# Optimization experiments

Hardware: AMD Instinct MI355X
Metric: run time of the kernel (lower is better)

## Reference

```python
import jax, jax.numpy as jnp
import numpy as np

DIM = 768; DEPTH = 4; HEADS = 12; DHEAD = 64; INNER = HEADS * DHEAD; FF = 4 * DIM
CHUNK = 64; ROTD = 32  # rotary_emb_dim = max(dim_head//2, 32); freqs dim = ROTD (16 freqs duplicated)
B = 2; N = 2048; K = 32; R = 2; CN = 128


def _rotary(seq_len, offset=0):
    inv_freq = 1.0 / (10000.0 ** (jnp.arange(0, ROTD, 2, dtype=jnp.float32) / ROTD))
    pos = jnp.arange(seq_len, dtype=jnp.float32) + offset
    fr = pos[:, None] * inv_freq[None, :]
    return jnp.concatenate([fr, fr], axis=-1)  # (seq_len, ROTD)


def _rope(t, freqs):
    # t: (b, h, n, DHEAD); freqs: (n, rd). Rotate first rd dims, pass the rest.
    rd = freqs.shape[-1]
    t1, t2 = t[..., :rd], t[..., rd:]
    half = rd // 2
    rot = jnp.concatenate([-t1[..., half:], t1[..., :half]], axis=-1)
    return jnp.concatenate([t1 * jnp.cos(freqs) + rot * jnp.sin(freqs), t2], axis=-1)


def _rmsnorm(x, gamma, eps=1e-8):
    n = jnp.linalg.norm(x, axis=-1, keepdims=True) * (x.shape[-1] ** -0.5)
    return x / jnp.maximum(n, eps) * gamma


def _attn(x, gamma, wq, wkv, wo, bo, q_freqs, k_freqs, causal, context=None, mask=None):
    xn = _rmsnorm(x, gamma)
    kv_in = xn if context is None else context
    b = x.shape[0]
    q = (xn @ wq).reshape(b, -1, HEADS, DHEAD).transpose(0, 2, 1, 3)
    k, v = jnp.split(kv_in @ wkv, 2, axis=-1)
    k = k.reshape(b, -1, HEADS, DHEAD).transpose(0, 2, 1, 3)
    v = v.reshape(b, -1, HEADS, DHEAD).transpose(0, 2, 1, 3)
    q = q * (DHEAD ** -0.5)
    q = _rope(q, q_freqs)
    k = _rope(k, k_freqs)
    sim = jnp.einsum('bhid,bhjd->bhij', q, k)
    neg = -jnp.finfo(sim.dtype).max
    if mask is not None:
        sim = jnp.where(mask[:, None, None, :], sim, neg)
    if causal:
        i, j = sim.shape[-2], sim.shape[-1]
        cm = jnp.arange(j)[None, :] > (jnp.arange(i)[:, None] + (j - i))
        sim = jnp.where(cm, neg, sim)
    attn = jax.nn.softmax(sim, axis=-1)
    out = jnp.einsum('bhij,bhjd->bhid', attn, v)
    out = out.transpose(0, 2, 1, 3).reshape(b, -1, INNER)
    return out @ wo + bo


def _forward(x, retrieved, context_mask, attn_gamma, attn_wq, attn_wkv, attn_wo, attn_bo,
             ca_gamma, ca_wq, ca_wkv, ca_wo, ca_bo, ff_gamma, ff_w1, ff_b1, ff_w2, ff_b2, final_gamma):
    b, n = x.shape[0], x.shape[1]
    k_chunks, r, cn = retrieved.shape[1], retrieved.shape[2], retrieved.shape[3]
    seq_chunk = n // k_chunks  # == CHUNK
    pad = CHUNK - 1

    self_freqs = _rotary(n)
    # cross-attn q pos emb: rotary(seq_chunk, offset=CHUNK-1) then F.pad (-pad, pad)
    qf = _rotary(seq_chunk, offset=pad)
    qf = jnp.concatenate([qf[pad:], jnp.zeros((pad, ROTD), qf.dtype)], axis=0)  # (seq_chunk, ROTD)
    kf = jnp.tile(_rotary(cn), (r, 1))  # (r*cn, ROTD)

    ctx = retrieved.reshape(b * k_chunks, r * cn, DIM)
    cmask = context_mask.reshape(b * k_chunks, r * cn)

    for l in range(DEPTH):
        # causal self-attention with RoPE
        x = _attn(x, attn_gamma[l], attn_wq[l], attn_wkv[l], attn_wo[l], attn_bo[l],
                  self_freqs, self_freqs, True) + x
        # chunked cross-attention
        xs = jnp.concatenate([x[:, pad:], jnp.zeros((b, pad, DIM), x.dtype)], axis=1)
        xs = xs.reshape(b * k_chunks, seq_chunk, DIM)
        co = _attn(xs, ca_gamma[l], ca_wq[l], ca_wkv[l], ca_wo[l], ca_bo[l],
                   qf, kf, False, context=ctx, mask=cmask)
        co = co.reshape(b, n, DIM)
        co = jnp.concatenate([jnp.zeros((b, pad, DIM), co.dtype), co[:, :-pad]], axis=1)
        x = co + x
        # feed-forward (RMSNorm -> Linear -> GELU -> Linear)
        h = _rmsnorm(x, ff_gamma[l])
        h = jax.nn.gelu(h @ ff_w1[l] + ff_b1[l], approximate=False)
        x = (h @ ff_w2[l] + ff_b2[l]) + x

    return _rmsnorm(x, final_gamma)


def setup_inputs() -> dict:
    key = jax.random.key(0)
    ks = jax.random.split(key, 16)
    s = 0.02
    inp = {
        'x': jax.random.normal(ks[0], (B, N, DIM), jnp.float32),
        'retrieved': jax.random.normal(ks[1], (B, K, R, CN, DIM), jnp.float32),
        'context_mask': jnp.ones((B, K, R, CN), jnp.bool_),
        'attn_gamma': jnp.ones((DEPTH, DIM), jnp.float32),
        'attn_wq': s * jax.random.normal(ks[2], (DEPTH, DIM, INNER), jnp.float32),
        'attn_wkv': s * jax.random.normal(ks[3], (DEPTH, DIM, 2 * INNER), jnp.float32),
        'attn_wo': s * jax.random.normal(ks[4], (DEPTH, INNER, DIM), jnp.float32),
        'attn_bo': jnp.zeros((DEPTH, DIM), jnp.float32),
        'ca_gamma': jnp.ones((DEPTH, DIM), jnp.float32),
        'ca_wq': s * jax.random.normal(ks[5], (DEPTH, DIM, INNER), jnp.float32),
        'ca_wkv': s * jax.random.normal(ks[6], (DEPTH, DIM, 2 * INNER), jnp.float32),
        'ca_wo': s * jax.random.normal(ks[7], (DEPTH, INNER, DIM), jnp.float32),
        'ca_bo': jnp.zeros((DEPTH, DIM), jnp.float32),
        'ff_gamma': jnp.ones((DEPTH, DIM), jnp.float32),
        'ff_w1': s * jax.random.normal(ks[8], (DEPTH, DIM, FF), jnp.float32),
        'ff_b1': jnp.zeros((DEPTH, FF), jnp.float32),
        'ff_w2': s * jax.random.normal(ks[9], (DEPTH, FF, DIM), jnp.float32),
        'ff_b2': jnp.zeros((DEPTH, DIM), jnp.float32),
        'final_gamma': jnp.ones((DIM,), jnp.float32),
    }
    return inp


def reference(x, retrieved, context_mask, attn_gamma, attn_wq, attn_wkv, attn_wo, attn_bo,
              ca_gamma, ca_wq, ca_wkv, ca_wo, ca_bo, ff_gamma, ff_w1, ff_b1, ff_w2, ff_b2, final_gamma):
    return _forward(x, retrieved, context_mask, attn_gamma, attn_wq, attn_wkv, attn_wo, attn_bo,
                    ca_gamma, ca_wq, ca_wkv, ca_wo, ca_bo, ff_gamma, ff_w1, ff_b1, ff_w2, ff_b2, final_gamma)
```

## Files before the change

kernel.cpp:

```cpp
#include <hip/hip_runtime.h>


#define DIM 768
#define DEPTH 4
#define HEADS 12
#define DHEAD 64
#define INNER 768
#define FF 3072
#define NSEQ 2048
#define BB 2
#define NROWS 4096
#define CTXROWS 16384
#define PAD 63

typedef __attribute__((ext_vector_type(4))) float f32x4;
typedef __attribute__((ext_vector_type(16))) float f32x16;
typedef __attribute__((ext_vector_type(8))) short bf16x8;
typedef unsigned short ushort_t;

__device__ __forceinline__ ushort_t f2bf(float f) {
    union { float f; unsigned u; } c; c.f = f;
    unsigned r = c.u + 0x7fffu + ((c.u >> 16) & 1u);
    return (ushort_t)(r >> 16);
}
__device__ __forceinline__ float bf2f(ushort_t u) {
    return __uint_as_float(((unsigned)u) << 16);
}
__device__ __forceinline__ unsigned cvt_pk_bf16(float lo, float hi) {
    unsigned r;
    asm("v_cvt_pk_bf16_f32 %0, %1, %2" : "=v"(r) : "v"(lo), "v"(hi));
    return r;
}

__device__ __forceinline__ void gload16(const ushort_t* g, ushort_t* l) {
    __builtin_amdgcn_global_load_lds(
        (const __attribute__((address_space(1))) unsigned int*)g,
        (__attribute__((address_space(3))) unsigned int*)l,
        16, 0, 0);
}

__global__ __launch_bounds__(256) void f32_to_bf16_kernel(
    const float* __restrict__ in, ushort_t* __restrict__ out, long n)
{
    long i = ((long)blockIdx.x * 256 + threadIdx.x) * 4;
    if (i + 3 < n) {
        float4 v = *(const float4*)(in + i);
        unsigned long long pk =
            (unsigned long long)f2bf(v.x)
          | ((unsigned long long)f2bf(v.y) << 16)
          | ((unsigned long long)f2bf(v.z) << 32)
          | ((unsigned long long)f2bf(v.w) << 48);
        *(unsigned long long*)(out + i) = pk;
    }
}

__global__ __launch_bounds__(256) void rope_tab_kernel(float2* __restrict__ tbl)
{
    int idx = blockIdx.x * 256 + threadIdx.x;
    int pos = idx >> 4, dd = idx & 15;
    float inv = __expf(-(float)dd * 0.57564627324851f);
    float f = (float)pos * inv;
    float sn, cs;
    sincosf(f, &sn, &cs);
    tbl[idx] = make_float2(cs, sn);
}

__global__ __launch_bounds__(256) void transpose_all_kernel(
    const float* __restrict__ wq,  const float* __restrict__ wkv,
    const float* __restrict__ wo,  const float* __restrict__ cawq,
    const float* __restrict__ cawkv, const float* __restrict__ cawo,
    const float* __restrict__ w1,  const float* __restrict__ w2,
    ushort_t* __restrict__ WT, size_t perLayer)
{
    const size_t szQ = 768ULL * 768, szKV = 768ULL * 1536, szW1 = 768ULL * 3072;
    int t = blockIdx.x, l = blockIdx.y;
    const float* src; int K, N; size_t dstOff; int rel;
    if      (t < 576)  { src = wq;    K = 768;  N = 768;  dstOff = 0;                 rel = t; }
    else if (t < 1728) { src = wkv;   K = 768;  N = 1536; dstOff = szQ;               rel = t - 576; }
    else if (t < 2304) { src = wo;    K = 768;  N = 768;  dstOff = szQ + szKV;        rel = t - 1728; }
    else if (t < 2880) { src = cawq;  K = 768;  N = 768;  dstOff = szQ*2 + szKV;      rel = t - 2304; }
    else if (t < 4032) { src = cawkv; K = 768;  N = 1536; dstOff = szQ*3 + szKV;      rel = t - 2880; }
    else if (t < 4608) { src = cawo;  K = 768;  N = 768;  dstOff = szQ*3 + szKV*2;    rel = t - 4032; }
    else if (t < 6912) { src = w1;    K = 768;  N = 3072; dstOff = szQ*4 + szKV*2;    rel = t - 4608; }
    else               { src = w2;    K = 3072; N = 768;  dstOff = szQ*4 + szKV*2 + szW1; rel = t - 6912; }
    src += (size_t)l * K * N;
    ushort_t* dst = WT + (size_t)l * perLayer + dstOff;
    int tx = N >> 5;
    int bx = (rel % tx) * 32;
    int by = (rel / tx) * 32;

    __shared__ float tile[32][33];
    int cx = threadIdx.x & 31, cy = threadIdx.x >> 5;
    #pragma unroll
    for (int i = 0; i < 32; i += 8)
        tile[cy + i][cx] = src[(long)(by + cy + i) * N + bx + cx];
    __syncthreads();
    #pragma unroll
    for (int i = 0; i < 32; i += 8)
        dst[(long)(bx + cy + i) * K + by + cx] = f2bf(tile[cx][cy + i]);
}

__global__ __launch_bounds__(256) void vtrans_kernel(
    const ushort_t* __restrict__ src, long srcStride, long vOff,
    ushort_t* __restrict__ VT, int kPG)
{
    __shared__ __align__(16) ushort_t tile[64][72];
    const int rt = blockIdx.x;
    const int h = blockIdx.y;
    const int row0 = rt * 64;
    const int g = row0 / kPG;
    const int kb = row0 % kPG;
    const int t = threadIdx.x;
    const int r = t >> 2, q4 = (t & 3) * 16;

    const ushort_t* s = src + (long)(row0 + r) * srcStride + vOff + h * DHEAD + q4;
    *(uint4*)&tile[r][q4]     = *(const uint4*)s;
    *(uint4*)&tile[r][q4 + 8] = *(const uint4*)(s + 8);
    __syncthreads();

    ushort_t tmp[16];
    #pragma unroll
    for (int c = 0; c < 16; c++) tmp[c] = tile[q4 + c][r];
    ushort_t* dst = VT + (((long)(g * HEADS + h) * DHEAD + r) * kPG + kb + q4);
    *(uint4*)dst       = *(uint4*)&tmp[0];
    *(uint4*)(dst + 8) = *(uint4*)&tmp[8];
}

template<int MODE>
__global__ __launch_bounds__(256) void rmsnorm_kernel(
    const float* __restrict__ x, const float* __restrict__ gamma,
    void* __restrict__ out)
{
    int row = blockIdx.x;
    int t = threadIdx.x;
    long src = row;
    bool zero = false;
    if (MODE == 1) {
        int p = row & (NSEQ - 1);
        zero = (p + PAD) >= NSEQ;
        src = (long)row + PAD;
    }
    float v[3];
    #pragma unroll
    for (int i = 0; i < 3; i++)
        v[i] = zero ? 0.0f : x[src * DIM + t + i * 256];
    float ss = v[0]*v[0] + v[1]*v[1] + v[2]*v[2];
    #pragma unroll
    for (int s = 1; s < 64; s <<= 1) ss += __shfl_xor(ss, s);
    __shared__ float red[4];
    if ((t & 63) == 0) red[t >> 6] = ss;
    __syncthreads();
    ss = red[0] + red[1] + red[2] + red[3];
    float rms = sqrtf(ss * (1.0f / 768.0f));
    float scl = 1.0f / fmaxf(rms, 1e-8f);
    #pragma unroll
    for (int i = 0; i < 3; i++) {
        int e = t + i * 256;
        float ov = v[i] * scl * gamma[e];
        if (MODE == 2) ((float*)out)[(long)row * DIM + e] = ov;
        else           ((ushort_t*)out)[(long)row * DIM + e] = f2bf(ov);
    }
}

__device__ __forceinline__ void rope_row(
    const ushort_t* __restrict__ s, int pos, const float2* __restrict__ tbl,
    ushort_t* __restrict__ dst, float scale)
{
    for (int e = threadIdx.x; e < DIM; e += 256) {
        int d = e & 63;
        float v = bf2f(s[e]);
        float outv;
        if (d < 32 && pos >= 0) {
            float2 cs = tbl[pos * 16 + (d & 15)];
            float other = bf2f(s[e + ((d < 16) ? 16 : -16)]);
            outv = (d < 16) ? (v * cs.x - other * cs.y) : (v * cs.x + other * cs.y);
        } else outv = v;
        dst[e] = f2bf(outv * scale);
    }
}

__global__ __launch_bounds__(256) void rope_self_kernel(
    const ushort_t* __restrict__ qkv, const float2* __restrict__ tbl,
    ushort_t* __restrict__ Qb, ushort_t* __restrict__ Kh)
{
    int r = blockIdx.x;
    if (r < NROWS) {
        rope_row(qkv + (long)r * 2304, r & (NSEQ - 1), tbl,
                 Qb + (long)r * DIM, 0.125f);
    } else {
        int rr = r - NROWS;
        rope_row(qkv + (long)rr * 2304 + 768, rr & (NSEQ - 1), tbl,
                 Kh + (long)rr * DIM, 1.0f);
    }
}

__global__ __launch_bounds__(256) void rope_cca_kernel(
    const ushort_t* __restrict__ qtmp, const ushort_t* __restrict__ ctxkv,
    const float2* __restrict__ tbl,
    ushort_t* __restrict__ Qb, ushort_t* __restrict__ Kh)
{
    int r = blockIdx.x;
    if (r < NROWS) {
        int pos = ((r & 63) == 0) ? 126 : -1;
        rope_row(qtmp + (long)r * DIM, pos, tbl, Qb + (long)r * DIM, 0.125f);
    } else {
        int rr = r - NROWS;
        rope_row(ctxkv + (long)rr * 1536, rr & 127, tbl,
                 Kh + (long)rr * DIM, 1.0f);
    }
}

template<bool CAUSAL>
__global__ __launch_bounds__(256) void attn_mfma_kernel(
    const ushort_t* __restrict__ Qb,
    const ushort_t* __restrict__ Kb,
    const ushort_t* __restrict__ VT,
    ushort_t* __restrict__ O,
    int qPG, int kPG)
{
    __shared__ float mO[4 * 32 * 68];
    __shared__ float mL[4 * 32];
    const int tid = threadIdx.x;
    const int lane = tid & 63;
    const int wave = tid >> 6;
    const int l31 = lane & 31;
    const int hi = lane >> 5;
    int head, group, qtA;
    if (CAUSAL) {
        int hg = blockIdx.x % 24;
        head = hg % HEADS; group = hg / HEADS;
        qtA = blockIdx.x / 24;
    } else {
        head = blockIdx.y; group = blockIdx.z; qtA = blockIdx.x;
    }
    const long kRow0 = (long)group * kPG;
    const ushort_t* vtb = VT + ((long)(group * HEADS + head) * DHEAD) * kPG;

    const int nPh = CAUSAL ? 2 : 1;
    for (int ph = 0; ph < nPh; ++ph) {
        const int qt = (ph == 0) ? qtA : (qPG / 32 - 1 - qtA);
        const int qLocal = qt * 32;
        const long qRow0 = (long)group * qPG + qLocal;

        bf16x8 qf[4];
        #pragma unroll
        for (int dc = 0; dc < 4; dc++)
            qf[dc] = *(const bf16x8*)&Qb[(qRow0 + l31) * DIM
                                          + head * DHEAD + dc*16 + hi*8];

        f32x16 acc0 = {}, acc1 = {};
        float lsum = 0.0f;

        const int tiles = CAUSAL ? (qt + 1) : (kPG >> 5);
        for (int t = wave; t < tiles; t += 4) {
            const int t0 = t << 5;
            bf16x8 kf[4];
            #pragma unroll
            for (int dc = 0; dc < 4; dc++)
                kf[dc] = *(const bf16x8*)&Kb[(kRow0 + t0 + l31) * DIM
                                              + head * DHEAD + dc*16 + hi*8];
            f32x16 s = {};
            #pragma unroll
            for (int dc = 0; dc < 4; dc++)
                s = __builtin_amdgcn_mfma_f32_32x32x16_bf16(kf[dc], qf[dc], s, 0, 0, 0);

            if (CAUSAL && t == qt) {
                #pragma unroll
                for (int r = 0; r < 16; r++) {
                    int kg = t0 + (r & 3) + 8 * (r >> 2) + 4 * hi;
                    if (kg > qLocal + l31) s[r] = -1e30f;
                }
            }

            float p[16];
            #pragma unroll
            for (int r = 0; r < 16; r++) {
                p[r] = __expf(s[r] - 8.0f);
                lsum += p[r];
            }
            unsigned pr[8], pt[8];
            #pragma unroll
            for (int j = 0; j < 8; j++) pr[j] = cvt_pk_bf16(p[2*j], p[2*j+1]);
            #pragma unroll
            for (int j = 0; j < 8; j++) pt[j] = (unsigned)__shfl_xor((int)pr[j], 32);
            union { unsigned w[4]; bf16x8 v; } a0u, a1u;
            a0u.w[0] = hi ? pt[2] : pr[0];
            a0u.w[1] = hi ? pt[3] : pr[1];
            a0u.w[2] = hi ? pr[2] : pt[0];
            a0u.w[3] = hi ? pr[3] : pt[1];
            a1u.w[0] = hi ? pt[6] : pr[4];
            a1u.w[1] = hi ? pt[7] : pr[5];
            a1u.w[2] = hi ? pr[6] : pt[4];
            a1u.w[3] = hi ? pr[7] : pt[5];

            #pragma unroll
            for (int dh = 0; dh < 2; dh++) {
                const ushort_t* vrow = &vtb[(long)(dh*32 + l31) * kPG + t0 + hi*8];
                bf16x8 vf0 = *(const bf16x8*)vrow;
                bf16x8 vf1 = *(const bf16x8*)(vrow + 16);
                if (dh == 0) {
                    acc0 = __builtin_amdgcn_mfma_f32_32x32x16_bf16(a0u.v, vf0, acc0, 0, 0, 0);
                    acc0 = __builtin_amdgcn_mfma_f32_32x32x16_bf16(a1u.v, vf1, acc0, 0, 0, 0);
                } else {
                    acc1 = __builtin_amdgcn_mfma_f32_32x32x16_bf16(a0u.v, vf0, acc1, 0, 0, 0);
                    acc1 = __builtin_amdgcn_mfma_f32_32x32x16_bf16(a1u.v, vf1, acc1, 0, 0, 0);
                }
            }
        }

        lsum += __shfl_xor(lsum, 32);

        __syncthreads();
        #pragma unroll
        for (int r = 0; r < 16; r++) {
            int q = (r & 3) + 8 * (r >> 2) + 4 * hi;
            mO[wave*2176 + q*68 + l31]      = acc0[r];
            mO[wave*2176 + q*68 + 32 + l31] = acc1[r];
        }
        if (lane < 32) mL[wave*32 + lane] = lsum;
        __syncthreads();

        {
            const int row = tid >> 3;
            const int c0 = (tid & 7) * 8;
            float L = mL[row] + mL[32 + row] + mL[64 + row] + mL[96 + row];
            float inv = 1.0f / L;
            ushort_t ov[8];
            #pragma unroll
            for (int c = 0; c < 8; c++) {
                int col = c0 + c;
                float sv = mO[row*68 + col] + mO[2176 + row*68 + col]
                         + mO[2*2176 + row*68 + col] + mO[3*2176 + row*68 + col];
                ov[c] = f2bf(sv * inv);
            }
            *(uint4*)&O[(qRow0 + row) * DIM + head * DHEAD + c0] = *(uint4*)ov;
        }
    }
}

#define BM 128
#define BN 128
#define BK 32

template<int EPI>
__device__ __forceinline__ void gemm_epilogue(
    f32x4 (&acc)[4], void* Cout, const float* bias, const float* resid,
    long row0, long col0, int lane, int N)
{
    const int l15 = lane & 15;
    const int g4 = lane >> 4;
    #pragma unroll
    for (int j = 0; j < 4; j++) {
        long col = col0 + j * 16 + l15;
        float bv = (EPI & 2) ? bias[col] : 0.0f;
        #pragma unroll
        for (int r = 0; r < 4; r++) {
            long row = row0 + g4 * 4 + r;
            float v = acc[j][r] + bv;
            if (EPI & 8)
                v = 0.5f * v * (1.0f + erff(v * 0.70710678118655f));
            long orow = row;
            bool store = true;
            if (EPI & 16) {
                if ((row & (NSEQ - 1)) < NSEQ - PAD) orow = row + PAD;
                else store = false;
            }
            if (store) {
                if (EPI & 4) v += resid[orow * N + col];
                if (EPI & 1) ((ushort_t*)Cout)[orow * N + col] = f2bf(v);
                else         ((float*)Cout)[orow * N + col] = v;
            }
        }
    }
}

__device__ __forceinline__ int xcd_swz(int id, int nwg) {
    int q8 = nwg >> 3;
    return (id & 7) * q8 + (id >> 3);
}

template<int EPI>
__global__ __launch_bounds__(256) void gemm_bf16_kernel(
    const ushort_t* __restrict__ A, const ushort_t* __restrict__ Bt,
    void* __restrict__ Cout, const float* __restrict__ bias,
    const float* __restrict__ resid, int M, int N, int K, int gx)
{
    __shared__ __align__(16) ushort_t lA[2][BM * BK];
    __shared__ __align__(16) ushort_t lB[2][BN * BK];
    const int tid = threadIdx.x;
    const int lane = tid & 63;
    const int wave = tid >> 6;
    const int wg = xcd_swz(blockIdx.x, gridDim.x);
    const long bm = (long)(wg / gx) * BM;
    const long bn = (long)(wg % gx) * BN;
    const int wr = (wave >> 1) * 64;
    const int wc = (wave & 1) * 64;
    f32x4 acc[4][4] = {};

    const int sub = lane >> 2;
    const int gp  = lane & 3;
    const int swz = gp ^ (sub & 3) ^ ((sub >> 2) & 1);
    const ushort_t* gA0 = A  + (bm + wave*32 + sub) * (size_t)K + swz*8;
    const ushort_t* gA1 = gA0 + (size_t)16 * K;
    const ushort_t* gB0 = Bt + (bn + wave*32 + sub) * (size_t)K + swz*8;
    const ushort_t* gB1 = gB0 + (size_t)16 * K;
    const int oA0 = (wave*32) * BK;
    const int oA1 = (wave*32 + 16) * BK;

    const int nst = K / BK;
    gload16(gA0, &lA[0][oA0]);
    gload16(gA1, &lA[0][oA1]);
    gload16(gB0, &lB[0][oA0]);
    gload16(gB1, &lB[0][oA1]);
    __syncthreads();

    for (int t = 0; t < nst; ++t) {
        const int cur = t & 1;
        if (t + 1 < nst) {
            const int k0 = (t + 1) * BK;
            gload16(gA0 + k0, &lA[cur ^ 1][oA0]);
            gload16(gA1 + k0, &lA[cur ^ 1][oA1]);
            gload16(gB0 + k0, &lB[cur ^ 1][oA0]);
            gload16(gB1 + k0, &lB[cur ^ 1][oA1]);
        }

        bf16x8 af[4], bfr[4];
        const int g = lane >> 4;
        #pragma unroll
        for (int i = 0; i < 4; i++) {
            int r  = wr + i * 16 + (lane & 15);
            int rc = wc + i * 16 + (lane & 15);
            af[i]  = *(const bf16x8*)&lA[cur][r  * BK + ((g ^ (r  & 3) ^ ((r  >> 2) & 1)) * 8)];
            bfr[i] = *(const bf16x8*)&lB[cur][rc * BK + ((g ^ (rc & 3) ^ ((rc >> 2) & 1)) * 8)];
        }
        #pragma unroll
        for (int i = 0; i < 4; i++)
            #pragma unroll
            for (int j = 0; j < 4; j++)
                acc[i][j] = __builtin_amdgcn_mfma_f32_16x16x32_bf16(
                    af[i], bfr[j], acc[i][j], 0, 0, 0);

        __syncthreads();
    }

    #pragma unroll
    for (int i = 0; i < 4; i++)
        gemm_epilogue<EPI>(acc[i], Cout, bias, resid,
                           bm + wr + i * 16, bn + wc, lane, N);
}

template<int EPI>
__global__ __launch_bounds__(256) void gemm64_bf16_kernel(
    const ushort_t* __restrict__ A, const ushort_t* __restrict__ Bt,
    void* __restrict__ Cout, const float* __restrict__ bias,
    const float* __restrict__ resid, int M, int N, int K, int gx)
{
    __shared__ __align__(16) ushort_t lA[2][64 * 32];
    __shared__ __align__(16) ushort_t lB[2][128 * 32];
    const int tid = threadIdx.x;
    const int lane = tid & 63;
    const int wave = tid >> 6;
    const int wg = xcd_swz(blockIdx.x, gridDim.x);
    const long bm = (long)(wg / gx) * 64;
    const long bn = (long)(wg % gx) * 128;
    const int wr = (wave >> 1) * 32;
    const int wc = (wave & 1) * 64;
    f32x4 acc[2][4] = {};

    const int sub = lane >> 2;
    const int gp  = lane & 3;
    const int swz = gp ^ (sub & 3) ^ ((sub >> 2) & 1);
    const int s0 = wave * 3, s1 = s0 + 1, s2 = s0 + 2;
    const bool a0 = s0 < 4, a1 = s1 < 4, a2 = s2 < 4;
    const ushort_t* g0 = (a0 ? A + (bm + s0*16 + sub) * (size_t)K
                             : Bt + (bn + (s0-4)*16 + sub) * (size_t)K) + swz*8;
    const ushort_t* g1 = (a1 ? A + (bm + s1*16 + sub) * (size_t)K
                             : Bt + (bn + (s1-4)*16 + sub) * (size_t)K) + swz*8;
    const ushort_t* g2 = (a2 ? A + (bm + s2*16 + sub) * (size_t)K
                             : Bt + (bn + (s2-4)*16 + sub) * (size_t)K) + swz*8;
    const int o0 = (a0 ? s0 : s0 - 4) * 16 * 32;
    const int o1 = (a1 ? s1 : s1 - 4) * 16 * 32;
    const int o2 = (a2 ? s2 : s2 - 4) * 16 * 32;

    const int nst = K / 32;
    gload16(g0, a0 ? &lA[0][o0] : &lB[0][o0]);
    gload16(g1, a1 ? &lA[0][o1] : &lB[0][o1]);
    gload16(g2, a2 ? &lA[0][o2] : &lB[0][o2]);
    __syncthreads();

    for (int t = 0; t < nst; ++t) {
        const int cur = t & 1;
        if (t + 1 < nst) {
            const int k0 = (t + 1) * 32;
            const int nb = cur ^ 1;
            gload16(g0 + k0, a0 ? &lA[nb][o0] : &lB[nb][o0]);
            gload16(g1 + k0, a1 ? &lA[nb][o1] : &lB[nb][o1]);
            gload16(g2 + k0, a2 ? &lA[nb][o2] : &lB[nb][o2]);
        }

        bf16x8 af[2], bfr[4];
        const int g = lane >> 4;
        #pragma unroll
        for (int i = 0; i < 2; i++) {
            int r = wr + i * 16 + (lane & 15);
            af[i] = *(const bf16x8*)&lA[cur][r * 32 + ((g ^ (r & 3) ^ ((r >> 2) & 1)) * 8)];
        }
        #pragma unroll
        for (int j = 0; j < 4; j++) {
            int rc = wc + j * 16 + (lane & 15);
            bfr[j] = *(const bf16x8*)&lB[cur][rc * 32 + ((g ^ (rc & 3) ^ ((rc >> 2) & 1)) * 8)];
        }
        #pragma unroll
        for (int i = 0; i < 2; i++)
            #pragma unroll
            for (int j = 0; j < 4; j++)
                acc[i][j] = __builtin_amdgcn_mfma_f32_16x16x32_bf16(
                    af[i], bfr[j], acc[i][j], 0, 0, 0);

        __syncthreads();
    }

    #pragma unroll
    for (int i = 0; i < 2; i++)
        gemm_epilogue<EPI>(acc[i], Cout, bias, resid,
                           bm + wr + i * 16, bn + wc, lane, N);
}

extern "C" void kernel_launch(void* const* d_in, const int* in_sizes, int n_in,
                              void* d_out, int out_size, void* d_ws, size_t ws_size,
                              hipStream_t stream) {
    const float* in_x       = (const float*)d_in[0];
    const float* retrieved  = (const float*)d_in[1];
    const float* attn_gamma = (const float*)d_in[3];
    const float* attn_wq    = (const float*)d_in[4];
    const float* attn_wkv   = (const float*)d_in[5];
    const float* attn_wo    = (const float*)d_in[6];
    const float* attn_bo    = (const float*)d_in[7];
    const float* ca_gamma   = (const float*)d_in[8];
    const float* ca_wq      = (const float*)d_in[9];
    const float* ca_wkv     = (const float*)d_in[10];
    const float* ca_wo      = (const float*)d_in[11];
    const float* ca_bo      = (const float*)d_in[12];
    const float* ff_gamma   = (const float*)d_in[13];
    const float* ff_w1      = (const float*)d_in[14];
    const float* ff_b1      = (const float*)d_in[15];
    const float* ff_w2      = (const float*)d_in[16];
    const float* ff_b2      = (const float*)d_in[17];
    const float* fin_gamma  = (const float*)d_in[18];

    float* x = (float*)d_out;

    char* p = (char*)d_ws;
    auto alloc = [&](size_t bytes) {
        char* r = p; p += (bytes + 255) & ~(size_t)255; return r;
    };
    const size_t szQ = 768ULL * 768, szKV = 768ULL * 1536, szW1 = 768ULL * 3072;
    const size_t perLayer = szQ * 4 + szKV * 2 + szW1 * 2;
    ushort_t* WT     = (ushort_t*)alloc(DEPTH * perLayer * 2);
    ushort_t* ctx_bf = (ushort_t*)alloc((size_t)CTXROWS * DIM * 2);
    ushort_t* xn_bf  = (ushort_t*)alloc((size_t)NROWS * DIM * 2);
    ushort_t* qtmp   = (ushort_t*)alloc((size_t)NROWS * DIM * 2);
    ushort_t* qkv    = (ushort_t*)alloc((size_t)NROWS * 2304 * 2);
    ushort_t* ctxkv  = (ushort_t*)alloc((size_t)CTXROWS * 1536 * 2);
    ushort_t* Qb     = (ushort_t*)alloc((size_t)NROWS * DIM * 2);
    ushort_t* Kh     = (ushort_t*)alloc((size_t)CTXROWS * DIM * 2);
    ushort_t* attn_o = (ushort_t*)alloc((size_t)NROWS * DIM * 2);
    ushort_t* VT     = (ushort_t*)alloc((size_t)64 * HEADS * DHEAD * 256 * 2);
    float2*   tbl    = (float2*)alloc((size_t)NSEQ * 16 * sizeof(float2));
    ushort_t* hgelu  = ctxkv;

    hipMemcpyAsync(x, in_x, (size_t)NROWS * DIM * 4, hipMemcpyDeviceToDevice, stream);
    f32_to_bf16_kernel<<<CTXROWS * DIM / 1024, 256, 0, stream>>>(
        retrieved, ctx_bf, (long)CTXROWS * DIM);
    rope_tab_kernel<<<NSEQ * 16 / 256, 256, 0, stream>>>(tbl);
    transpose_all_kernel<<<dim3(9216, DEPTH), 256, 0, stream>>>(
        attn_wq, attn_wkv, attn_wo, ca_wq, ca_wkv, ca_wo, ff_w1, ff_w2,
        WT, perLayer);

    for (int l = 0; l < DEPTH; l++) {
        ushort_t* base   = WT + (size_t)l * perLayer;
        ushort_t* wq_t    = base;
        ushort_t* wkv_t   = wq_t + szQ;
        ushort_t* wo_t    = wkv_t + szKV;
        ushort_t* cawq_t  = wo_t + szQ;
        ushort_t* cawkv_t = cawq_t + szQ;
        ushort_t* cawo_t  = cawkv_t + szKV;
        ushort_t* w1_t    = cawo_t + szQ;
        ushort_t* w2_t    = w1_t + szW1;

        rmsnorm_kernel<0><<<NROWS, 256, 0, stream>>>(x, attn_gamma + l*DIM, xn_bf);
        gemm_bf16_kernel<1><<<18 * 32, 256, 0, stream>>>(
            xn_bf, wq_t, qkv, nullptr, nullptr, NROWS, 2304, 768, 18);
        rope_self_kernel<<<NROWS * 2, 256, 0, stream>>>(qkv, tbl, Qb, Kh);
        vtrans_kernel<<<dim3(NROWS / 64, HEADS), 256, 0, stream>>>(
            qkv, 2304, 1536, VT, NSEQ);
        attn_mfma_kernel<true><<<dim3(32 * 24), 256, 0, stream>>>(
            Qb, Kh, VT, attn_o, NSEQ, NSEQ);
        gemm64_bf16_kernel<6><<<6 * 64, 256, 0, stream>>>(
            attn_o, wo_t, x, attn_bo + l*DIM, x, NROWS, 768, 768, 6);

        rmsnorm_kernel<1><<<NROWS, 256, 0, stream>>>(x, ca_gamma + l*DIM, xn_bf);
        gemm64_bf16_kernel<1><<<6 * 64, 256, 0, stream>>>(
            xn_bf, cawq_t, qtmp, nullptr, nullptr, NROWS, 768, 768, 6);
        gemm_bf16_kernel<1><<<12 * 128, 256, 0, stream>>>(
            ctx_bf, cawkv_t, ctxkv, nullptr, nullptr, CTXROWS, 1536, 768, 12);
        rope_cca_kernel<<<NROWS + CTXROWS, 256, 0, stream>>>(qtmp, ctxkv, tbl, Qb, Kh);
        vtrans_kernel<<<dim3(CTXROWS / 64, HEADS), 256, 0, stream>>>(
            ctxkv, 1536, 768, VT, 256);
        attn_mfma_kernel<false><<<dim3(2, HEADS, 64), 256, 0, stream>>>(
            Qb, Kh, VT, attn_o, 64, 256);
        gemm64_bf16_kernel<22><<<6 * 64, 256, 0, stream>>>(
            attn_o, cawo_t, x, ca_bo + l*DIM, x, NROWS, 768, 768, 6);

        rmsnorm_kernel<0><<<NROWS, 256, 0, stream>>>(x, ff_gamma + l*DIM, xn_bf);
        gemm_bf16_kernel<11><<<24 * 32, 256, 0, stream>>>(
            xn_bf, w1_t, hgelu, ff_b1 + l*FF, nullptr, NROWS, FF, 768, 24);
        gemm64_bf16_kernel<6><<<6 * 64, 256, 0, stream>>>(
            hgelu, w2_t, x, ff_b2 + l*DIM, x, NROWS, 768, FF, 6);
    }

    rmsnorm_kernel<2><<<NROWS, 256, 0, stream>>>(x, fin_gamma, d_out);
}
```

Baseline: 1.505 ms.

## Fuse RoPE, scaling and V transpose into projection GEMM epilogues

The QKV and cross-attention Q/KV projection GEMMs now write rotary-embedded, scaled Q/K and transposed V straight into the attention layouts from their epilogues. This removes the separate rope and vtrans kernels and the intermediate qkv/qtmp/ctxkv buffers. The weight transpose kernel also switches to 64x64 tiles with float4 loads and 16-byte bf16 stores. In exchange, the epilogue uses narrow scattered stores and depends on each 64-column tile lining up with one head.

```diff
diff --git a/kernel.cpp b/kernel.cpp
--- a/kernel.cpp
+++ b/kernel.cpp
@@ -75,55 +75,40 @@
     const size_t szQ = 768ULL * 768, szKV = 768ULL * 1536, szW1 = 768ULL * 3072;
     int t = blockIdx.x, l = blockIdx.y;
     const float* src; int K, N; size_t dstOff; int rel;
-    if      (t < 576)  { src = wq;    K = 768;  N = 768;  dstOff = 0;                 rel = t; }
-    else if (t < 1728) { src = wkv;   K = 768;  N = 1536; dstOff = szQ;               rel = t - 576; }
-    else if (t < 2304) { src = wo;    K = 768;  N = 768;  dstOff = szQ + szKV;        rel = t - 1728; }
-    else if (t < 2880) { src = cawq;  K = 768;  N = 768;  dstOff = szQ*2 + szKV;      rel = t - 2304; }
-    else if (t < 4032) { src = cawkv; K = 768;  N = 1536; dstOff = szQ*3 + szKV;      rel = t - 2880; }
-    else if (t < 4608) { src = cawo;  K = 768;  N = 768;  dstOff = szQ*3 + szKV*2;    rel = t - 4032; }
-    else if (t < 6912) { src = w1;    K = 768;  N = 3072; dstOff = szQ*4 + szKV*2;    rel = t - 4608; }
-    else               { src = w2;    K = 3072; N = 768;  dstOff = szQ*4 + szKV*2 + szW1; rel = t - 6912; }
+    if      (t < 144)  { src = wq;    K = 768;  N = 768;  dstOff = 0;                 rel = t; }
+    else if (t < 432)  { src = wkv;   K = 768;  N = 1536; dstOff = szQ;               rel = t - 144; }
+    else if (t < 576)  { src = wo;    K = 768;  N = 768;  dstOff = szQ + szKV;        rel = t - 432; }
+    else if (t < 720)  { src = cawq;  K = 768;  N = 768;  dstOff = szQ*2 + szKV;      rel = t - 576; }
+    else if (t < 1008) { src = cawkv; K = 768;  N = 1536; dstOff = szQ*3 + szKV;      rel = t - 720; }
+    else if (t < 1152) { src = cawo;  K = 768;  N = 768;  dstOff = szQ*3 + szKV*2;    rel = t - 1008; }
+    else if (t < 1728) { src = w1;    K = 768;  N = 3072; dstOff = szQ*4 + szKV*2;    rel = t - 1152; }
+    else               { src = w2;    K = 3072; N = 768;  dstOff = szQ*4 + szKV*2 + szW1; rel = t - 1728; }
     src += (size_t)l * K * N;
     ushort_t* dst = WT + (size_t)l * perLayer + dstOff;
-    int tx = N >> 5;
-    int bx = (rel % tx) * 32;
-    int by = (rel / tx) * 32;
-
-    __shared__ float tile[32][33];
-    int cx = threadIdx.x & 31, cy = threadIdx.x >> 5;
-    #pragma unroll
-    for (int i = 0; i < 32; i += 8)
-        tile[cy + i][cx] = src[(long)(by + cy + i) * N + bx + cx];
+    int tx = N >> 6;
+    int bx = (rel % tx) * 64;
+    int by = (rel / tx) * 64;
+
+    __shared__ ushort_t tile[64][70];
+    const int r = threadIdx.x >> 2;
+    const int cq = (threadIdx.x & 3) * 16;
+    const float* s = src + (long)(by + r) * N + bx + cq;
+    #pragma unroll
+    for (int c = 0; c < 16; c += 4) {
+        float4 v = *(const float4*)(s + c);
+        tile[r][cq + c + 0] = f2bf(v.x);
+        tile[r][cq + c + 1] = f2bf(v.y);
+        tile[r][cq + c + 2] = f2bf(v.z);
+        tile[r][cq + c + 3] = f2bf(v.w);
+    }
     __syncthreads();
-    #pragma unroll
-    for (int i = 0; i < 32; i += 8)
-        dst[(long)(bx + cy + i) * K + by + cx] = f2bf(tile[cx][cy + i]);
-}
-
-__global__ __launch_bounds__(256) void vtrans_kernel(
-    const ushort_t* __restrict__ src, long srcStride, long vOff,
-    ushort_t* __restrict__ VT, int kPG)
-{
-    __shared__ __align__(16) ushort_t tile[64][72];
-    const int rt = blockIdx.x;
-    const int h = blockIdx.y;
-    const int row0 = rt * 64;
-    const int g = row0 / kPG;
-    const int kb = row0 % kPG;
-    const int t = threadIdx.x;
-    const int r = t >> 2, q4 = (t & 3) * 16;
-
-    const ushort_t* s = src + (long)(row0 + r) * srcStride + vOff + h * DHEAD + q4;
-    *(uint4*)&tile[r][q4]     = *(const uint4*)s;
-    *(uint4*)&tile[r][q4 + 8] = *(const uint4*)(s + 8);
-    __syncthreads();
-
-    ushort_t tmp[16];
-    #pragma unroll
-    for (int c = 0; c < 16; c++) tmp[c] = tile[q4 + c][r];
-    ushort_t* dst = VT + (((long)(g * HEADS + h) * DHEAD + r) * kPG + kb + q4);
-    *(uint4*)dst       = *(uint4*)&tmp[0];
-    *(uint4*)(dst + 8) = *(uint4*)&tmp[8];
+
+    ushort_t pk[16];
+    #pragma unroll
+    for (int c = 0; c < 16; c++) pk[c] = tile[cq + c][r];
+    ushort_t* d = dst + (long)(bx + r) * K + by + cq;
+    *(uint4*)d       = *(uint4*)&pk[0];
+    *(uint4*)(d + 8) = *(uint4*)&pk[8];
 }
 
 template<int MODE>
@@ -159,54 +144,6 @@
         float ov = v[i] * scl * gamma[e];
         if (MODE == 2) ((float*)out)[(long)row * DIM + e] = ov;
         else           ((ushort_t*)out)[(long)row * DIM + e] = f2bf(ov);
-    }
-}
-
-__device__ __forceinline__ void rope_row(
-    const ushort_t* __restrict__ s, int pos, const float2* __restrict__ tbl,
-    ushort_t* __restrict__ dst, float scale)
-{
-    for (int e = threadIdx.x; e < DIM; e += 256) {
-        int d = e & 63;
-        float v = bf2f(s[e]);
-        float outv;
-        if (d < 32 && pos >= 0) {
-            float2 cs = tbl[pos * 16 + (d & 15)];
-            float other = bf2f(s[e + ((d < 16) ? 16 : -16)]);
-            outv = (d < 16) ? (v * cs.x - other * cs.y) : (v * cs.x + other * cs.y);
-        } else outv = v;
-        dst[e] = f2bf(outv * scale);
-    }
-}
-
-__global__ __launch_bounds__(256) void rope_self_kernel(
-    const ushort_t* __restrict__ qkv, const float2* __restrict__ tbl,
-    ushort_t* __restrict__ Qb, ushort_t* __restrict__ Kh)
-{
-    int r = blockIdx.x;
-    if (r < NROWS) {
-        rope_row(qkv + (long)r * 2304, r & (NSEQ - 1), tbl,
-                 Qb + (long)r * DIM, 0.125f);
-    } else {
-        int rr = r - NROWS;
-        rope_row(qkv + (long)rr * 2304 + 768, rr & (NSEQ - 1), tbl,
-                 Kh + (long)rr * DIM, 1.0f);
-    }
-}
-
-__global__ __launch_bounds__(256) void rope_cca_kernel(
-    const ushort_t* __restrict__ qtmp, const ushort_t* __restrict__ ctxkv,
-    const float2* __restrict__ tbl,
-    ushort_t* __restrict__ Qb, ushort_t* __restrict__ Kh)
-{
-    int r = blockIdx.x;
-    if (r < NROWS) {
-        int pos = ((r & 63) == 0) ? 126 : -1;
-        rope_row(qtmp + (long)r * DIM, pos, tbl, Qb + (long)r * DIM, 0.125f);
-    } else {
-        int rr = r - NROWS;
-        rope_row(ctxkv + (long)rr * 1536, rr & 127, tbl,
-                 Kh + (long)rr * DIM, 1.0f);
     }
 }
 
@@ -338,20 +275,74 @@
     }
 }
 
-#define BM 128
-#define BN 128
-#define BK 32
-
 template<int EPI>
 __device__ __forceinline__ void gemm_epilogue(
     f32x4 (&acc)[4], void* Cout, const float* bias, const float* resid,
-    long row0, long col0, int lane, int N)
+    long row0, long colBase, int lane, int N,
+    ushort_t* Qb, ushort_t* Kh, ushort_t* VT, const float2* tbl)
 {
     const int l15 = lane & 15;
     const int g4 = lane >> 4;
+
+    if (EPI & (32 | 64)) {
+        const long vstart = (EPI & 32) ? 1536 : 768;
+        if (colBase >= vstart) {
+            const int kPG = (EPI & 32) ? 2048 : 256;
+            const int h = (int)((colBase - vstart) >> 6);
+            const long grp = row0 / kPG;
+            const long krow = (row0 & (kPG - 1)) + g4 * 4;
+            #pragma unroll
+            for (int j = 0; j < 4; j++) {
+                int d = j * 16 + l15;
+                ushort_t pk[4];
+                #pragma unroll
+                for (int r = 0; r < 4; r++) pk[r] = f2bf(acc[j][r]);
+                *(unsigned long long*)&VT[((grp * HEADS + h) * DHEAD + d) * kPG + krow]
+                    = *(unsigned long long*)pk;
+            }
+            return;
+        }
+        const bool isQ = (EPI & 32) && (colBase < 768);
+        const float scale = isQ ? 0.125f : 1.0f;
+        ushort_t* dst = isQ ? Qb : Kh;
+        const long dcol = isQ ? colBase : (colBase - 768);
+        #pragma unroll
+        for (int r = 0; r < 4; r++) {
+            long row = row0 + g4 * 4 + r;
+            int pos = (EPI & 32) ? (int)(row & (NSEQ - 1)) : (int)(row & 127);
+            float2 cs = tbl[pos * 16 + l15];
+            float v0 = acc[0][r], v1 = acc[1][r];
+            float o0 = v0 * cs.x - v1 * cs.y;
+            float o1 = v1 * cs.x + v0 * cs.y;
+            ushort_t* drow = dst + row * DIM + dcol;
+            drow[l15]      = f2bf(o0 * scale);
+            drow[16 + l15] = f2bf(o1 * scale);
+            drow[32 + l15] = f2bf(acc[2][r] * scale);
+            drow[48 + l15] = f2bf(acc[3][r] * scale);
+        }
+        return;
+    }
+    if (EPI & 128) {
+        #pragma unroll
+        for (int r = 0; r < 4; r++) {
+            long row = row0 + g4 * 4 + r;
+            float2 cs = ((row & 63) == 0) ? tbl[126 * 16 + l15]
+                                          : make_float2(1.0f, 0.0f);
+            float v0 = acc[0][r], v1 = acc[1][r];
+            float o0 = v0 * cs.x - v1 * cs.y;
+            float o1 = v1 * cs.x + v0 * cs.y;
+            ushort_t* drow = Qb + row * DIM + colBase;
+            drow[l15]      = f2bf(o0 * 0.125f);
+            drow[16 + l15] = f2bf(o1 * 0.125f);
+            drow[32 + l15] = f2bf(acc[2][r] * 0.125f);
+            drow[48 + l15] = f2bf(acc[3][r] * 0.125f);
+        }
+        return;
+    }
+
     #pragma unroll
     for (int j = 0; j < 4; j++) {
-        long col = col0 + j * 16 + l15;
+        long col = colBase + j * 16 + l15;
         float bv = (EPI & 2) ? bias[col] : 0.0f;
         #pragma unroll
         for (int r = 0; r < 4; r++) {
@@ -379,11 +370,16 @@
     return (id & 7) * q8 + (id >> 3);
 }
 
+#define BM 128
+#define BN 128
+#define BK 32
+
 template<int EPI>
 __global__ __launch_bounds__(256) void gemm_bf16_kernel(
     const ushort_t* __restrict__ A, const ushort_t* __restrict__ Bt,
     void* __restrict__ Cout, const float* __restrict__ bias,
-    const float* __restrict__ resid, int M, int N, int K, int gx)
+    const float* __restrict__ resid, int M, int N, int K, int gx,
+    ushort_t* Qb, ushort_t* Kh, ushort_t* VT, const float2* tbl)
 {
     __shared__ __align__(16) ushort_t lA[2][BM * BK];
     __shared__ __align__(16) ushort_t lB[2][BN * BK];
@@ -446,14 +442,15 @@
     #pragma unroll
     for (int i = 0; i < 4; i++)
         gemm_epilogue<EPI>(acc[i], Cout, bias, resid,
-                           bm + wr + i * 16, bn + wc, lane, N);
+                           bm + wr + i * 16, bn + wc, lane, N, Qb, Kh, VT, tbl);
 }
 
 template<int EPI>
 __global__ __launch_bounds__(256) void gemm64_bf16_kernel(
     const ushort_t* __restrict__ A, const ushort_t* __restrict__ Bt,
     void* __restrict__ Cout, const float* __restrict__ bias,
-    const float* __restrict__ resid, int M, int N, int K, int gx)
+    const float* __restrict__ resid, int M, int N, int K, int gx,
+    ushort_t* Qb, ushort_t* Kh, ushort_t* VT, const float2* tbl)
 {
     __shared__ __align__(16) ushort_t lA[2][64 * 32];
     __shared__ __align__(16) ushort_t lB[2][128 * 32];
@@ -523,7 +520,7 @@
     #pragma unroll
     for (int i = 0; i < 2; i++)
         gemm_epilogue<EPI>(acc[i], Cout, bias, resid,
-                           bm + wr + i * 16, bn + wc, lane, N);
+                           bm + wr + i * 16, bn + wc, lane, N, Qb, Kh, VT, tbl);
 }
 
 extern "C" void kernel_launch(void* const* d_in, const int* in_sizes, int n_in,
@@ -559,21 +556,18 @@
     ushort_t* WT     = (ushort_t*)alloc(DEPTH * perLayer * 2);
     ushort_t* ctx_bf = (ushort_t*)alloc((size_t)CTXROWS * DIM * 2);
     ushort_t* xn_bf  = (ushort_t*)alloc((size_t)NROWS * DIM * 2);
-    ushort_t* qtmp   = (ushort_t*)alloc((size_t)NROWS * DIM * 2);
-    ushort_t* qkv    = (ushort_t*)alloc((size_t)NROWS * 2304 * 2);
-    ushort_t* ctxkv  = (ushort_t*)alloc((size_t)CTXROWS * 1536 * 2);
     ushort_t* Qb     = (ushort_t*)alloc((size_t)NROWS * DIM * 2);
     ushort_t* Kh     = (ushort_t*)alloc((size_t)CTXROWS * DIM * 2);
     ushort_t* attn_o = (ushort_t*)alloc((size_t)NROWS * DIM * 2);
     ushort_t* VT     = (ushort_t*)alloc((size_t)64 * HEADS * DHEAD * 256 * 2);
+    ushort_t* hgelu  = (ushort_t*)alloc((size_t)NROWS * FF * 2);
     float2*   tbl    = (float2*)alloc((size_t)NSEQ * 16 * sizeof(float2));
-    ushort_t* hgelu  = ctxkv;
 
     hipMemcpyAsync(x, in_x, (size_t)NROWS * DIM * 4, hipMemcpyDeviceToDevice, stream);
     f32_to_bf16_kernel<<<CTXROWS * DIM / 1024, 256, 0, stream>>>(
         retrieved, ctx_bf, (long)CTXROWS * DIM);
     rope_tab_kernel<<<NSEQ * 16 / 256, 256, 0, stream>>>(tbl);
-    transpose_all_kernel<<<dim3(9216, DEPTH), 256, 0, stream>>>(
+    transpose_all_kernel<<<dim3(2304, DEPTH), 256, 0, stream>>>(
         attn_wq, attn_wkv, attn_wo, ca_wq, ca_wkv, ca_wo, ff_w1, ff_w2,
         WT, perLayer);
 
@@ -589,34 +583,35 @@
         ushort_t* w2_t    = w1_t + szW1;
 
         rmsnorm_kernel<0><<<NROWS, 256, 0, stream>>>(x, attn_gamma + l*DIM, xn_bf);
-        gemm_bf16_kernel<1><<<18 * 32, 256, 0, stream>>>(
-            xn_bf, wq_t, qkv, nullptr, nullptr, NROWS, 2304, 768, 18);
-        rope_self_kernel<<<NROWS * 2, 256, 0, stream>>>(qkv, tbl, Qb, Kh);
-        vtrans_kernel<<<dim3(NROWS / 64, HEADS), 256, 0, stream>>>(
-            qkv, 2304, 1536, VT, NSEQ);
+        gemm_bf16_kernel<32><<<18 * 32, 256, 0, stream>>>(
+            xn_bf, wq_t, nullptr, nullptr, nullptr, NROWS, 2304, 768, 18,
+            Qb, Kh, VT, tbl);
         attn_mfma_kernel<true><<<dim3(32 * 24), 256, 0, stream>>>(
             Qb, Kh, VT, attn_o, NSEQ, NSEQ);
         gemm64_bf16_kernel<6><<<6 * 64, 256, 0, stream>>>(
-            attn_o, wo_t, x, attn_bo + l*DIM, x, NROWS, 768, 768, 6);
+            attn_o, wo_t, x, attn_bo + l*DIM, x, NROWS, 768, 768, 6,
+            nullptr, nullptr, nullptr, nullptr);
 
         rmsnorm_kernel<1><<<NROWS, 256, 0, stream>>>(x, ca_gamma + l*DIM, xn_bf);
-        gemm64_bf16_kernel<1><<<6 * 64, 256, 0, stream>>>(
-            xn_bf, cawq_t, qtmp, nullptr, nullptr, NROWS, 768, 768, 6);
-        gemm_bf16_kernel<1><<<12 * 128, 256, 0, stream>>>(
-            ctx_bf, cawkv_t, ctxkv, nullptr, nullptr, CTXROWS, 1536, 768, 12);
-        rope_cca_kernel<<<NROWS + CTXROWS, 256, 0, stream>>>(qtmp, ctxkv, tbl, Qb, Kh);
-        vtrans_kernel<<<dim3(CTXROWS / 64, HEADS), 256, 0, stream>>>(
-            ctxkv, 1536, 768, VT, 256);
+        gemm64_bf16_kernel<128><<<6 * 64, 256, 0, stream>>>(
+            xn_bf, cawq_t, nullptr, nullptr, nullptr, NROWS, 768, 768, 6,
+            Qb, nullptr, nullptr, tbl);
+        gemm_bf16_kernel<64><<<12 * 128, 256, 0, stream>>>(
+            ctx_bf, cawkv_t, nullptr, nullptr, nullptr, CTXROWS, 1536, 768, 12,
+            nullptr, Kh, VT, tbl);
         attn_mfma_kernel<false><<<dim3(2, HEADS, 64), 256, 0, stream>>>(
             Qb, Kh, VT, attn_o, 64, 256);
         gemm64_bf16_kernel<22><<<6 * 64, 256, 0, stream>>>(
-            attn_o, cawo_t, x, ca_bo + l*DIM, x, NROWS, 768, 768, 6);
+            attn_o, cawo_t, x, ca_bo + l*DIM, x, NROWS, 768, 768, 6,
+            nullptr, nullptr, nullptr, nullptr);
 
         rmsnorm_kernel<0><<<NROWS, 256, 0, stream>>>(x, ff_gamma + l*DIM, xn_bf);
         gemm_bf16_kernel<11><<<24 * 32, 256, 0, stream>>>(
-            xn_bf, w1_t, hgelu, ff_b1 + l*FF, nullptr, NROWS, FF, 768, 24);
+            xn_bf, w1_t, hgelu, ff_b1 + l*FF, nullptr, NROWS, FF, 768, 24,
+            nullptr, nullptr, nullptr, nullptr);
         gemm64_bf16_kernel<6><<<6 * 64, 256, 0, stream>>>(
-            hgelu, w2_t, x, ff_b2 + l*DIM, x, NROWS, 768, FF, 6);
+            hgelu, w2_t, x, ff_b2 + l*DIM, x, NROWS, 768, FF, 6,
+            nullptr, nullptr, nullptr, nullptr);
     }
 
     rmsnorm_kernel<2><<<NROWS, 256, 0, stream>>>(x, fin_gamma, d_out);
```

Result: faster. 1.305 ms (-13.3%).
